# Optimization experiments

Hardware: AMD Instinct MI355X
Metric: run time of the kernel (lower is better)

## Reference

```python
import jax, jax.numpy as jnp
import numpy as np

N0 = 1373      # hardcoded node-type split in the original forward
TAO = 0.4
EPS = 1e-12


def _l2norm(x, axis):
    # matches torch F.normalize(p=2): x / max(||x||, eps)
    n = jnp.sqrt(jnp.sum(x * x, axis=axis, keepdims=True))
    return x / jnp.maximum(n, EPS)


def setup_inputs() -> dict:
    key = jax.random.key(0)
    ks = jax.random.split(key, 12)
    N, E, D_IN, F, H, D = 20000, 320000, 256, 32, 8, 32
    feat = jax.random.normal(ks[0], (N, D_IN), jnp.float32)
    sloc = jax.random.normal(ks[1], (N, D), jnp.float32)
    topo_fea = jax.random.normal(ks[2], (N, D), jnp.float32)
    src = jax.random.randint(ks[3], (E,), 0, N)
    dst = jax.random.randint(ks[4], (E,), 0, N)
    e_feat = jax.random.randint(ks[5], (E,), 0, 4)
    s = 1.0 / np.sqrt(D_IN)
    W_proj0 = jax.random.normal(ks[6], (D_IN, H * F), jnp.float32) * s
    W_proj1 = jax.random.normal(ks[7], (D_IN, H * F), jnp.float32) * s
    W_prob = jax.random.normal(ks[8], (H, F, F), jnp.float32) * (1.0 / np.sqrt(F))
    W_res0 = jax.random.normal(ks[9], (D_IN, H * F), jnp.float32) * s
    W_res1 = jax.random.normal(ks[10], (D_IN, H * F), jnp.float32) * s
    etype_attn = jnp.ones((4,), jnp.float32)
    return dict(feat=feat, sloc=sloc, topo_fea=topo_fea, src=src, dst=dst,
                e_feat=e_feat, W_proj0=W_proj0, W_proj1=W_proj1, W_prob=W_prob,
                W_res0=W_res0, W_res1=W_res1, etype_attn=etype_attn)


def reference(feat, sloc, topo_fea, src, dst, e_feat,
              W_proj0, W_proj1, W_prob, W_res0, W_res1, etype_attn):
    N = feat.shape[0]
    H, F = W_prob.shape[0], W_prob.shape[2]
    sloc3 = sloc[:, None, :]        # (N,1,D) -- .unsqueeze(1)
    topo3 = topo_fea[:, None, :]

    # per-type node projection
    feat_src = jnp.concatenate(
        [feat[:N0] @ W_proj0, feat[N0:] @ W_proj1], axis=0).reshape(N, H, F)
    # per-head attention feature: softmax(tanh(fc4prob_i(.)), dim=feat)
    ft_attn = jax.nn.softmax(
        jnp.tanh(jnp.einsum('nhf,hfg->nhg', feat_src, W_prob)), axis=2)
    # F.normalize over the NODE dimension (dim=0), as in original
    ft_norm = _l2norm(feat_src, axis=0)

    sloc_n = _l2norm(sloc3, axis=2)
    topo_n = _l2norm(topo3, axis=2)

    # edge attention scores
    a = jnp.sum(ft_attn[dst] * ft_norm[src], axis=2, keepdims=True)   # (E,H,1)
    cos_s = jnp.sum(sloc_n[src] * sloc_n[dst], axis=2, keepdims=True)  # (E,1,1)
    cos_t = jnp.sum(topo_n[src] * topo_n[dst], axis=2, keepdims=True)
    sim = (TAO * cos_s + (1.0 - TAO) * cos_t + 1.0) / 2.0             # (E,1,1)
    e = (sim * a * etype_attn[e_feat][:, None, None])[:, :, 0]        # (E,H)

    # edge softmax: segment softmax over incoming edges of each dst node
    m = jax.ops.segment_max(e, dst, num_segments=N)                   # (N,H)
    ex = jnp.exp(e - m[dst])
    z = jax.ops.segment_sum(ex, dst, num_segments=N)
    att = ex / z[dst]                                                 # (E,H)

    # three u_mul_e + sum aggregations
    aw = att[:, :, None]                                              # (E,H,1)
    rst = jax.ops.segment_sum(feat_src[src] * aw, dst, num_segments=N)  # (N,H,F)
    sl2 = jax.ops.segment_sum(sloc3[src] * aw, dst, num_segments=N)     # (N,H,D)
    tp2 = jax.ops.segment_sum(topo3[src] * aw, dst, num_segments=N)     # (N,H,D)

    resval = jnp.concatenate(
        [feat[:N0] @ W_res0, feat[N0:] @ W_res1], axis=0).reshape(N, H, F)
    out_fea = jax.nn.relu(rst + resval).mean(axis=1)   # (N,F)
    out_sloc = (sl2 + sloc3).mean(axis=1)              # (N,D)
    out_topo = (tp2 + topo3).mean(axis=1)              # (N,D)
    return out_fea, out_sloc, out_topo
```

## Files before the change

kernel.cpp:

```cpp
#include <hip/hip_runtime.h>
#include <math.h>

#define HN0 1373
#define BM 128
#define BN 128
#define BK 32
#define LDT 40

typedef __attribute__((ext_vector_type(8))) short short8;
typedef __attribute__((ext_vector_type(4))) float f32x4;

__device__ inline unsigned short f2bf(float f) {
  unsigned int u = __float_as_uint(f);
  unsigned int r = (u + 0x7FFFu + ((u >> 16) & 1u)) >> 16;
  return (unsigned short)r;
}
__device__ inline float bflo(unsigned int u) { return __uint_as_float(u << 16); }
__device__ inline float bfhi(unsigned int u) { return __uint_as_float(u & 0xFFFF0000u); }

__device__ inline uint4 pack8bf(float4 a, float4 b) {
  uint4 o;
  o.x = (unsigned)f2bf(a.x) | ((unsigned)f2bf(a.y) << 16);
  o.y = (unsigned)f2bf(a.z) | ((unsigned)f2bf(a.w) << 16);
  o.z = (unsigned)f2bf(b.x) | ((unsigned)f2bf(b.y) << 16);
  o.w = (unsigned)f2bf(b.z) | ((unsigned)f2bf(b.w) << 16);
  return o;
}

__global__ __launch_bounds__(256) void prep(
    const float* __restrict__ Wp0, const float* __restrict__ Wr0,
    const float* __restrict__ Wp1, const float* __restrict__ Wr1,
    unsigned short* __restrict__ BTw,
    const float* __restrict__ sloc, const float* __restrict__ topo,
    unsigned short* __restrict__ slt, unsigned short* __restrict__ sltn,
    const int* __restrict__ dst, int* __restrict__ deg, int N, int E) {
  __shared__ float T[64][72];
  int b = blockIdx.x;
  int tid = threadIdx.x;
  int nodeBlocks = (N + 7) / 8;
  if (b < 64) {
    int mat = b >> 4;
    int t16 = b & 15;
    int kT = (t16 & 3) * 64;
    int nT = (t16 >> 2) * 64;
    const float* W = (mat == 0) ? Wp0 : (mat == 1) ? Wr0 : (mat == 2) ? Wp1 : Wr1;
    int g = mat >> 1;
    int nbase = (mat & 1) * 256;
    int r = tid >> 2;
    int cb = (tid & 3) * 16;
    const float* srcp = W + (size_t)(kT + r) * 256 + nT + cb;
#pragma unroll
    for (int q = 0; q < 4; ++q) {
      float4 v = *reinterpret_cast<const float4*>(srcp + q * 4);
      T[cb + q * 4 + 0][r] = v.x;
      T[cb + q * 4 + 1][r] = v.y;
      T[cb + q * 4 + 2][r] = v.z;
      T[cb + q * 4 + 3][r] = v.w;
    }
    __syncthreads();
    int nl = tid >> 2;
    int kb = (tid & 3) * 16;
    unsigned int pk[8];
#pragma unroll
    for (int q = 0; q < 8; ++q) {
      unsigned short lo = f2bf(T[nl][kb + q * 2]);
      unsigned short hi = f2bf(T[nl][kb + q * 2 + 1]);
      pk[q] = (unsigned)lo | ((unsigned)hi << 16);
    }
    unsigned short* dstp = BTw + (size_t)g * 512 * 256 + (size_t)(nbase + nT + nl) * 256 + kT + kb;
    *reinterpret_cast<uint4*>(dstp) = make_uint4(pk[0], pk[1], pk[2], pk[3]);
    *reinterpret_cast<uint4*>(dstp + 8) = make_uint4(pk[4], pk[5], pk[6], pk[7]);
  } else if (b < 64 + nodeBlocks) {
    int node = (b - 64) * 8 + (tid >> 5);
    int d = tid & 31;
    if (node >= N) return;
    float s = sloc[(size_t)node * 32 + d];
    float t = topo[(size_t)node * 32 + d];
    float ss = s * s, tt = t * t;
#pragma unroll
    for (int m = 16; m >= 1; m >>= 1) {
      ss += __shfl_xor(ss, m);
      tt += __shfl_xor(tt, m);
    }
    float is = 1.f / fmaxf(sqrtf(ss), 1e-12f);
    float it = 1.f / fmaxf(sqrtf(tt), 1e-12f);
    slt[(size_t)node * 64 + d] = f2bf(s);
    slt[(size_t)node * 64 + 32 + d] = f2bf(t);
    sltn[(size_t)node * 64 + d] = f2bf(s * is);
    sltn[(size_t)node * 64 + 32 + d] = f2bf(t * it);
  } else {
    int e = (b - 64 - nodeBlocks) * 256 + tid;
    if (e < E) atomicAdd(&deg[dst[e]], 1);
  }
}

__global__ __launch_bounds__(256) void gemm_mfma(
    const float* __restrict__ A, const unsigned short* __restrict__ BTw,
    unsigned short* __restrict__ feat_bf, unsigned short* __restrict__ resval,
    int N) {
  __shared__ __align__(16) unsigned short As[BM * LDT];
  __shared__ __align__(16) unsigned short Bs[BN * LDT];
  int tid = threadIdx.x;
  int lane = tid & 63;
  int w = tid >> 6;
  int wr = w >> 1, wc = w & 1;

  int g0t = (HN0 + BM - 1) / BM;
  int bx = blockIdx.x;
  bool g1 = bx >= g0t;
  int rowBase = g1 ? HN0 + (bx - g0t) * BM : bx * BM;
  int rowEnd = g1 ? N : HN0;
  const unsigned short* BT = BTw + (g1 ? (size_t)512 * 256 : 0);
  int colBase = blockIdx.y * BN;

  int r0 = tid >> 2;
  int kp = (tid & 3) << 3;
  int ar1 = min(rowBase + r0, rowEnd - 1);
  int ar2 = min(rowBase + r0 + 64, rowEnd - 1);
  const float* aP1 = A + (size_t)ar1 * 256 + kp;
  const float* aP2 = A + (size_t)ar2 * 256 + kp;
  const unsigned short* bP1 = BT + (size_t)(colBase + r0) * 256 + kp;
  const unsigned short* bP2 = bP1 + (size_t)64 * 256;
  int wo1 = r0 * LDT + kp;
  int wo2 = (r0 + 64) * LDT + kp;

  int q = lane >> 4;
  int fr = lane & 15;
  int aOff = (wr * 64 + fr) * LDT + q * 8;
  int bOff = (wc * 64 + fr) * LDT + q * 8;

  f32x4 acc[4][4] = {};

  float4 fa1a = *reinterpret_cast<const float4*>(aP1);
  float4 fa1b = *reinterpret_cast<const float4*>(aP1 + 4);
  float4 fa2a = *reinterpret_cast<const float4*>(aP2);
  float4 fa2b = *reinterpret_cast<const float4*>(aP2 + 4);
  uint4 rb1 = *reinterpret_cast<const uint4*>(bP1);
  uint4 rb2 = *reinterpret_cast<const uint4*>(bP2);

  for (int t = 0; t < 8; ++t) {
    *reinterpret_cast<uint4*>(&As[wo1]) = pack8bf(fa1a, fa1b);
    *reinterpret_cast<uint4*>(&As[wo2]) = pack8bf(fa2a, fa2b);
    *reinterpret_cast<uint4*>(&Bs[wo1]) = rb1;
    *reinterpret_cast<uint4*>(&Bs[wo2]) = rb2;
    __syncthreads();
    if (t < 7) {
      int ko = (t + 1) * BK;
      fa1a = *reinterpret_cast<const float4*>(aP1 + ko);
      fa1b = *reinterpret_cast<const float4*>(aP1 + ko + 4);
      fa2a = *reinterpret_cast<const float4*>(aP2 + ko);
      fa2b = *reinterpret_cast<const float4*>(aP2 + ko + 4);
      rb1 = *reinterpret_cast<const uint4*>(bP1 + ko);
      rb2 = *reinterpret_cast<const uint4*>(bP2 + ko);
    }
    short8 af[4], bf4[4];
#pragma unroll
    for (int i = 0; i < 4; ++i) {
      af[i] = *reinterpret_cast<const short8*>(&As[aOff + i * 16 * LDT]);
      bf4[i] = *reinterpret_cast<const short8*>(&Bs[bOff + i * 16 * LDT]);
    }
#pragma unroll
    for (int i = 0; i < 4; ++i)
#pragma unroll
      for (int j = 0; j < 4; ++j)
        acc[i][j] = __builtin_amdgcn_mfma_f32_16x16x32_bf16(af[i], bf4[j], acc[i][j], 0, 0, 0);
    __syncthreads();
  }

  unsigned short* outp = (colBase < 256) ? feat_bf : resval;
  int cOff = colBase & 255;
#pragma unroll
  for (int i = 0; i < 4; ++i) {
    int rb = rowBase + wr * 64 + i * 16 + q * 4;
#pragma unroll
    for (int j = 0; j < 4; ++j) {
      int col = cOff + wc * 64 + j * 16 + fr;
      f32x4 v = acc[i][j];
#pragma unroll
      for (int rr = 0; rr < 4; ++rr) {
        int r = rb + rr;
        if (r < rowEnd) outp[(size_t)r * 256 + col] = f2bf(v[rr]);
      }
    }
  }
}

__global__ __launch_bounds__(256) void attn_probs(
    const unsigned short* __restrict__ feat_bf, const float* __restrict__ W_prob,
    unsigned short* __restrict__ ft_attn, float* __restrict__ col_ss, int N) {
  __shared__ float fsL[16 * 256];
  int tid = threadIdx.x;
  int h = tid >> 5, g = tid & 31;
  float wreg[32];
#pragma unroll
  for (int f = 0; f < 32; ++f) wreg[f] = W_prob[h * 1024 + f * 32 + g];
  int nodeBase = blockIdx.x * 16;
  float ssp = 0.f;
  for (int i = 0; i < 16; ++i) {
    int n = nodeBase + i;
    float v = (n < N) ? __uint_as_float((unsigned)feat_bf[(size_t)n * 256 + tid] << 16) : 0.f;
    fsL[i * 256 + tid] = v;
    ssp += v * v;
  }
  atomicAdd(&col_ss[tid], ssp);
  __syncthreads();
  for (int i = 0; i < 16; ++i) {
    int n = nodeBase + i;
    if (n >= N) break;
    const float* fr = &fsL[i * 256 + h * 32];
    float t = 0.f;
#pragma unroll
    for (int f = 0; f < 32; ++f) t = fmaf(fr[f], wreg[f], t);
    float e2 = __expf(2.f * t);
    t = 1.f - 2.f * __builtin_amdgcn_rcpf(e2 + 1.f);
    float ex = __expf(t);
    float sm = ex;
#pragma unroll
    for (int s = 16; s >= 1; s >>= 1) sm += __shfl_xor(sm, s);
    ft_attn[(size_t)n * 256 + tid] = f2bf(ex * __builtin_amdgcn_rcpf(sm));
  }
}

__global__ __launch_bounds__(512) void scan_block(const int* __restrict__ deg,
                                                  int* __restrict__ start,
                                                  int* __restrict__ bsum, int n) {
  __shared__ int buf[512];
  int tid = threadIdx.x;
  int gid = blockIdx.x * 512 + tid;
  int v = (gid < n) ? deg[gid] : 0;
  buf[tid] = v;
  __syncthreads();
  for (int off = 1; off < 512; off <<= 1) {
    int t = (tid >= off) ? buf[tid - off] : 0;
    __syncthreads();
    buf[tid] += t;
    __syncthreads();
  }
  if (gid < n) start[gid] = buf[tid] - v;
  if (tid == 511) bsum[blockIdx.x] = buf[511];
}

__global__ __launch_bounds__(256) void mid_small(float* __restrict__ col_ss,
                                                 int* __restrict__ bsum, int nb) {
  int tid = threadIdx.x;
  col_ss[tid] = 1.f / fmaxf(sqrtf(col_ss[tid]), 1e-12f);
  __shared__ int buf[128];
  if (tid < nb) buf[tid] = bsum[tid];
  __syncthreads();
  if (tid == 0) {
    int run = 0;
    for (int i = 0; i < nb; ++i) { int v = buf[i]; buf[i] = run; run += v; }
  }
  __syncthreads();
  if (tid < nb) bsum[tid] = buf[tid];
}

__global__ __launch_bounds__(256) void fill_sim(
    const int* __restrict__ src, const int* __restrict__ dst,
    const int* __restrict__ e_feat, const float* __restrict__ etype_attn,
    const unsigned short* __restrict__ sltn,
    const int* __restrict__ start, const int* __restrict__ bsum,
    int* __restrict__ cursor, int2* __restrict__ csr, int E) {
  int tid = threadIdx.x;
  int j = tid & 3;
  int e = blockIdx.x * 64 + (tid >> 2);
  if (e >= E) return;
  int s = src[e], d = dst[e];
  const unsigned short* ps = sltn + (size_t)s * 64 + j * 16;
  const unsigned short* pd = sltn + (size_t)d * 64 + j * 16;
  uint4 a0 = *reinterpret_cast<const uint4*>(ps);
  uint4 a1 = *reinterpret_cast<const uint4*>(ps + 8);
  uint4 b0 = *reinterpret_cast<const uint4*>(pd);
  uint4 b1 = *reinterpret_cast<const uint4*>(pd + 8);
  float u = bflo(a0.x) * bflo(b0.x) + bfhi(a0.x) * bfhi(b0.x) +
            bflo(a0.y) * bflo(b0.y) + bfhi(a0.y) * bfhi(b0.y) +
            bflo(a0.z) * bflo(b0.z) + bfhi(a0.z) * bfhi(b0.z) +
            bflo(a0.w) * bflo(b0.w) + bfhi(a0.w) * bfhi(b0.w) +
            bflo(a1.x) * bflo(b1.x) + bfhi(a1.x) * bfhi(b1.x) +
            bflo(a1.y) * bflo(b1.y) + bfhi(a1.y) * bfhi(b1.y) +
            bflo(a1.z) * bflo(b1.z) + bfhi(a1.z) * bfhi(b1.z) +
            bflo(a1.w) * bflo(b1.w) + bfhi(a1.w) * bfhi(b1.w);
  u *= (j < 2) ? 0.4f : 0.6f;
  u += __shfl_xor(u, 1);
  u += __shfl_xor(u, 2);
  if (j == 0) {
    float sim = fmaf(u, 0.5f, 0.5f);
    float wv = sim * etype_attn[e_feat[e]];
    int pos = start[d] + bsum[d >> 9] + atomicAdd(&cursor[d], 1);
    csr[pos] = make_int2(s, __float_as_int(wv));
  }
}

#define LOADIDX(K, V, W)                                                       \
  do {                                                                         \
    int2 c_ = csr[s0 + (K)];                                                   \
    V = c_.x;                                                                  \
    W = __int_as_float(c_.y);                                                  \
  } while (0)

#define GATHER(V, FP, SL, TP)                                                  \
  do {                                                                         \
    FP = *reinterpret_cast<const uint2*>(feat_bf + (size_t)(V) * 256 + fb);    \
    const unsigned short* sp_ = slt + (size_t)(V) * 64 + db;                   \
    SL = *reinterpret_cast<const uint2*>(sp_);                                 \
    TP = *reinterpret_cast<const uint2*>(sp_ + 32);                            \
  } while (0)

#define CONSUME(W, FP, SL, TP)                                                 \
  do {                                                                         \
    float fs0 = bflo(FP.x), fs1 = bfhi(FP.x);                                  \
    float fs2 = bflo(FP.y), fs3 = bfhi(FP.y);                                  \
    float pa = ai4.x * fs0 + ai4.y * fs1 + ai4.z * fs2 + ai4.w * fs3;          \
    pa += __shfl_xor(pa, 1);                                                   \
    pa += __shfl_xor(pa, 2);                                                   \
    pa += __shfl_xor(pa, 4);                                                   \
    float p = __expf(pa * (W));                                                \
    l += p;                                                                    \
    accf.x = fmaf(p, fs0, accf.x); accf.y = fmaf(p, fs1, accf.y);              \
    accf.z = fmaf(p, fs2, accf.z); accf.w = fmaf(p, fs3, accf.w);              \
    accs.x = fmaf(p, bflo(SL.x), accs.x); accs.y = fmaf(p, bfhi(SL.x), accs.y);\
    accs.z = fmaf(p, bflo(SL.y), accs.z); accs.w = fmaf(p, bfhi(SL.y), accs.w);\
    acct.x = fmaf(p, bflo(TP.x), acct.x); acct.y = fmaf(p, bfhi(TP.x), acct.y);\
    acct.z = fmaf(p, bflo(TP.y), acct.z); acct.w = fmaf(p, bfhi(TP.y), acct.w);\
  } while (0)

__global__ __launch_bounds__(128) void edge_aggregate(
    const unsigned short* __restrict__ feat_bf, const unsigned short* __restrict__ resval,
    const unsigned short* __restrict__ ft_attn, const float* __restrict__ inv_cn,
    const unsigned short* __restrict__ slt,
    const float* __restrict__ sloc, const float* __restrict__ topo,
    const int* __restrict__ start, const int* __restrict__ bsum,
    const int* __restrict__ deg, const int2* __restrict__ csr,
    float* __restrict__ out, int N) {
  int wave = threadIdx.x >> 6;
  int n = blockIdx.x * 2 + wave;
  if (n >= N) return;
  int lane = threadIdx.x & 63;
  int j = lane & 7;
  int fb = (lane >> 3) * 32 + j * 4;
  int db = j * 4;

  uint2 at2 = *reinterpret_cast<const uint2*>(ft_attn + (size_t)n * 256 + fb);
  float4 icn4 = *reinterpret_cast<const float4*>(inv_cn + fb);
  float4 ai4 = make_float4(bflo(at2.x) * icn4.x, bfhi(at2.x) * icn4.y,
                           bflo(at2.y) * icn4.z, bfhi(at2.y) * icn4.w);
  float l = 0.f;
  float4 accf = make_float4(0.f, 0.f, 0.f, 0.f);
  float4 accs = make_float4(0.f, 0.f, 0.f, 0.f);
  float4 acct = make_float4(0.f, 0.f, 0.f, 0.f);
  int s0 = start[n] + bsum[n >> 9];
  int dg = deg[n];

  int vA = 0, vB = 0, vC = 0;
  float wA = 0.f, wB = 0.f, wC = 0.f;
  uint2 fpA = make_uint2(0u, 0u), fpB = make_uint2(0u, 0u), fpC = make_uint2(0u, 0u);
  uint2 slA = make_uint2(0u, 0u), slB = make_uint2(0u, 0u), slC = make_uint2(0u, 0u);
  uint2 tpA = make_uint2(0u, 0u), tpB = make_uint2(0u, 0u), tpC = make_uint2(0u, 0u);
  if (dg > 0) { LOADIDX(0, vA, wA); GATHER(vA, fpA, slA, tpA); }
  if (dg > 1) { LOADIDX(1, vB, wB); GATHER(vB, fpB, slB, tpB); }
  if (dg > 2) { LOADIDX(2, vC, wC); GATHER(vC, fpC, slC, tpC); }
  int i = 0;
  for (; i + 2 < dg; i += 3) {
    CONSUME(wA, fpA, slA, tpA);
    if (i + 3 < dg) { LOADIDX(i + 3, vA, wA); GATHER(vA, fpA, slA, tpA); }
    CONSUME(wB, fpB, slB, tpB);
    if (i + 4 < dg) { LOADIDX(i + 4, vB, wB); GATHER(vB, fpB, slB, tpB); }
    CONSUME(wC, fpC, slC, tpC);
    if (i + 5 < dg) { LOADIDX(i + 5, vC, wC); GATHER(vC, fpC, slC, tpC); }
  }
  if (i < dg) CONSUME(wA, fpA, slA, tpA);
  if (i + 1 < dg) CONSUME(wB, fpB, slB, tpB);

  float invl = (l > 0.f) ? 1.f / l : 0.f;

  uint2 res2 = *reinterpret_cast<const uint2*>(resval + (size_t)n * 256 + fb);
  float4 of = make_float4(fmaxf(fmaf(accf.x, invl, bflo(res2.x)), 0.f),
                          fmaxf(fmaf(accf.y, invl, bfhi(res2.x)), 0.f),
                          fmaxf(fmaf(accf.z, invl, bflo(res2.y)), 0.f),
                          fmaxf(fmaf(accf.w, invl, bfhi(res2.y)), 0.f));
  float4 os = make_float4(accs.x * invl, accs.y * invl, accs.z * invl, accs.w * invl);
  float4 ot = make_float4(acct.x * invl, acct.y * invl, acct.z * invl, acct.w * invl);
#pragma unroll
  for (int msk = 8; msk <= 32; msk <<= 1) {
    of.x += __shfl_xor(of.x, msk); of.y += __shfl_xor(of.y, msk);
    of.z += __shfl_xor(of.z, msk); of.w += __shfl_xor(of.w, msk);
    os.x += __shfl_xor(os.x, msk); os.y += __shfl_xor(os.y, msk);
    os.z += __shfl_xor(os.z, msk); os.w += __shfl_xor(os.w, msk);
    ot.x += __shfl_xor(ot.x, msk); ot.y += __shfl_xor(ot.y, msk);
    ot.w += __shfl_xor(ot.w, msk); ot.z += __shfl_xor(ot.z, msk);
  }
  if (lane < 8) {
    float4 sln = *reinterpret_cast<const float4*>(sloc + (size_t)n * 32 + db);
    float4 tpn = *reinterpret_cast<const float4*>(topo + (size_t)n * 32 + db);
    float4 o0 = make_float4(of.x * 0.125f, of.y * 0.125f, of.z * 0.125f, of.w * 0.125f);
    float4 o1 = make_float4(fmaf(os.x, 0.125f, sln.x), fmaf(os.y, 0.125f, sln.y),
                            fmaf(os.z, 0.125f, sln.z), fmaf(os.w, 0.125f, sln.w));
    float4 o2 = make_float4(fmaf(ot.x, 0.125f, tpn.x), fmaf(ot.y, 0.125f, tpn.y),
                            fmaf(ot.z, 0.125f, tpn.z), fmaf(ot.w, 0.125f, tpn.w));
    *reinterpret_cast<float4*>(out + (size_t)n * 32 + db) = o0;
    *reinterpret_cast<float4*>(out + (size_t)N * 32 + (size_t)n * 32 + db) = o1;
    *reinterpret_cast<float4*>(out + (size_t)2 * N * 32 + (size_t)n * 32 + db) = o2;
  }
}

extern "C" void kernel_launch(void* const* d_in, const int* in_sizes, int n_in,
                              void* d_out, int out_size, void* d_ws, size_t ws_size,
                              hipStream_t stream) {
  const float* feat = (const float*)d_in[0];
  const float* sloc = (const float*)d_in[1];
  const float* topo = (const float*)d_in[2];
  const int* src = (const int*)d_in[3];
  const int* dst = (const int*)d_in[4];
  const int* e_feat = (const int*)d_in[5];
  const float* W_proj0 = (const float*)d_in[6];
  const float* W_proj1 = (const float*)d_in[7];
  const float* W_prob = (const float*)d_in[8];
  const float* W_res0 = (const float*)d_in[9];
  const float* W_res1 = (const float*)d_in[10];
  const float* etype_attn = (const float*)d_in[11];
  int E = in_sizes[3];
  int N = in_sizes[1] / 32;
  float* out = (float*)d_out;

  char* ws = (char*)d_ws;
  size_t off = 0;
  auto alloc = [&](size_t bytes) -> char* {
    char* p = ws + off;
    off += (bytes + 255) & ~(size_t)255;
    return p;
  };
  int* deg = (int*)alloc((size_t)N * 4);
  int* cursor = (int*)alloc((size_t)N * 4);
  float* col_ss = (float*)alloc(256 * 4);
  size_t zeroBytes = ((char*)col_ss + 256 * 4) - (char*)deg;
  int* startArr = (int*)alloc(((size_t)N + 1) * 4);
  int* bsum = (int*)alloc(128 * 4);
  int2* csr = (int2*)alloc((size_t)E * 8);
  unsigned short* feat_bf = (unsigned short*)alloc((size_t)N * 256 * 2);
  unsigned short* slt = (unsigned short*)alloc((size_t)N * 64 * 2);
  unsigned short* sltn = (unsigned short*)alloc((size_t)N * 64 * 2);
  unsigned short* resval = (unsigned short*)alloc((size_t)N * 256 * 2);
  unsigned short* ft_attn = (unsigned short*)alloc((size_t)N * 256 * 2);
  unsigned short* BTw = (unsigned short*)alloc((size_t)2 * 512 * 256 * 2);

  hipMemsetAsync(deg, 0, zeroBytes, stream);

  int nodeBlocks = (N + 7) / 8;
  int degBlocks = (E + 255) / 256;
  prep<<<64 + nodeBlocks + degBlocks, 256, 0, stream>>>(
      W_proj0, W_res0, W_proj1, W_res1, BTw, sloc, topo, slt, sltn, dst, deg, N, E);

  int g0t = (HN0 + BM - 1) / BM;
  int g1t = (N - HN0 + BM - 1) / BM;
  gemm_mfma<<<dim3(g0t + g1t, 4), 256, 0, stream>>>(feat, BTw, feat_bf, resval, N);

  attn_probs<<<(N + 15) / 16, 256, 0, stream>>>(feat_bf, W_prob, ft_attn, col_ss, N);

  int nb = (N + 511) / 512;
  scan_block<<<nb, 512, 0, stream>>>(deg, startArr, bsum, N);
  mid_small<<<1, 256, 0, stream>>>(col_ss, bsum, nb);

  fill_sim<<<(E + 63) / 64, 256, 0, stream>>>(src, dst, e_feat, etype_attn, sltn,
                                              startArr, bsum, cursor, csr, E);

  edge_aggregate<<<(N + 1) / 2, 128, 0, stream>>>(feat_bf, resval, ft_attn, col_ss,
                                                  slt, sloc, topo, startArr, bsum,
                                                  deg, csr, out, N);
}
```

Measured before the change: 178.2 us.

## Fold degree scan into GEMM launch and block-sum scan into attention launch

Appends the per-block degree prefix scan (now 256-wide blocks) as extra blocks of the GEMM kernel, and the block-sum exclusive scan as an extra block of the attention-probability kernel. The column-norm reciprocal formerly computed in mid_small is now computed inline in edge_aggregate, and the attention dot product is split into four independent accumulators. This cuts two kernel launches and their serialization gaps, at the cost of redundant per-thread sqrt/reciprocal work and a larger bsum array. The GEMM grid is also flattened to 1D.

```diff
diff --git a/kernel.cpp b/kernel.cpp
--- a/kernel.cpp
+++ b/kernel.cpp
@@ -94,24 +94,43 @@
   }
 }
 
-__global__ __launch_bounds__(256) void gemm_mfma(
+__global__ __launch_bounds__(256) void gemm_scan(
     const float* __restrict__ A, const unsigned short* __restrict__ BTw,
     unsigned short* __restrict__ feat_bf, unsigned short* __restrict__ resval,
-    int N) {
+    const int* __restrict__ deg, int* __restrict__ start, int* __restrict__ bsum,
+    int G, int N) {
+  int b = blockIdx.x;
+  int tid = threadIdx.x;
+  if (b >= G) {
+    __shared__ int buf[256];
+    int b2 = b - G;
+    int gid = b2 * 256 + tid;
+    int v = (gid < N) ? deg[gid] : 0;
+    buf[tid] = v;
+    __syncthreads();
+    for (int off = 1; off < 256; off <<= 1) {
+      int t = (tid >= off) ? buf[tid - off] : 0;
+      __syncthreads();
+      buf[tid] += t;
+      __syncthreads();
+    }
+    if (gid < N) start[gid] = buf[tid] - v;
+    if (tid == 255) bsum[b2] = buf[255];
+    return;
+  }
   __shared__ __align__(16) unsigned short As[BM * LDT];
   __shared__ __align__(16) unsigned short Bs[BN * LDT];
-  int tid = threadIdx.x;
   int lane = tid & 63;
   int w = tid >> 6;
   int wr = w >> 1, wc = w & 1;
 
   int g0t = (HN0 + BM - 1) / BM;
-  int bx = blockIdx.x;
+  int bx = b >> 2;
+  int colBase = (b & 3) * BN;
   bool g1 = bx >= g0t;
   int rowBase = g1 ? HN0 + (bx - g0t) * BM : bx * BM;
   int rowEnd = g1 ? N : HN0;
   const unsigned short* BT = BTw + (g1 ? (size_t)512 * 256 : 0);
-  int colBase = blockIdx.y * BN;
 
   int r0 = tid >> 2;
   int kp = (tid & 3) << 3;
@@ -185,11 +204,24 @@
   }
 }
 
-__global__ __launch_bounds__(256) void attn_probs(
+__global__ __launch_bounds__(256) void attn_mid(
     const unsigned short* __restrict__ feat_bf, const float* __restrict__ W_prob,
-    unsigned short* __restrict__ ft_attn, float* __restrict__ col_ss, int N) {
+    unsigned short* __restrict__ ft_attn, float* __restrict__ col_ss,
+    int* __restrict__ bsum, int nb, int nAttn, int N) {
+  int tid = threadIdx.x;
+  if ((int)blockIdx.x >= nAttn) {
+    __shared__ int buf[128];
+    if (tid < nb) buf[tid] = bsum[tid];
+    __syncthreads();
+    if (tid == 0) {
+      int run = 0;
+      for (int i = 0; i < nb; ++i) { int v = buf[i]; buf[i] = run; run += v; }
+    }
+    __syncthreads();
+    if (tid < nb) bsum[tid] = buf[tid];
+    return;
+  }
   __shared__ float fsL[16 * 256];
-  int tid = threadIdx.x;
   int h = tid >> 5, g = tid & 31;
   float wreg[32];
 #pragma unroll
@@ -208,9 +240,15 @@
     int n = nodeBase + i;
     if (n >= N) break;
     const float* fr = &fsL[i * 256 + h * 32];
-    float t = 0.f;
-#pragma unroll
-    for (int f = 0; f < 32; ++f) t = fmaf(fr[f], wreg[f], t);
+    float t0 = 0.f, t1 = 0.f, t2 = 0.f, t3 = 0.f;
+#pragma unroll
+    for (int f = 0; f < 8; ++f) {
+      t0 = fmaf(fr[f * 4 + 0], wreg[f * 4 + 0], t0);
+      t1 = fmaf(fr[f * 4 + 1], wreg[f * 4 + 1], t1);
+      t2 = fmaf(fr[f * 4 + 2], wreg[f * 4 + 2], t2);
+      t3 = fmaf(fr[f * 4 + 3], wreg[f * 4 + 3], t3);
+    }
+    float t = (t0 + t1) + (t2 + t3);
     float e2 = __expf(2.f * t);
     t = 1.f - 2.f * __builtin_amdgcn_rcpf(e2 + 1.f);
     float ex = __expf(t);
@@ -219,40 +257,6 @@
     for (int s = 16; s >= 1; s >>= 1) sm += __shfl_xor(sm, s);
     ft_attn[(size_t)n * 256 + tid] = f2bf(ex * __builtin_amdgcn_rcpf(sm));
   }
-}
-
-__global__ __launch_bounds__(512) void scan_block(const int* __restrict__ deg,
-                                                  int* __restrict__ start,
-                                                  int* __restrict__ bsum, int n) {
-  __shared__ int buf[512];
-  int tid = threadIdx.x;
-  int gid = blockIdx.x * 512 + tid;
-  int v = (gid < n) ? deg[gid] : 0;
-  buf[tid] = v;
-  __syncthreads();
-  for (int off = 1; off < 512; off <<= 1) {
-    int t = (tid >= off) ? buf[tid - off] : 0;
-    __syncthreads();
-    buf[tid] += t;
-    __syncthreads();
-  }
-  if (gid < n) start[gid] = buf[tid] - v;
-  if (tid == 511) bsum[blockIdx.x] = buf[511];
-}
-
-__global__ __launch_bounds__(256) void mid_small(float* __restrict__ col_ss,
-                                                 int* __restrict__ bsum, int nb) {
-  int tid = threadIdx.x;
-  col_ss[tid] = 1.f / fmaxf(sqrtf(col_ss[tid]), 1e-12f);
-  __shared__ int buf[128];
-  if (tid < nb) buf[tid] = bsum[tid];
-  __syncthreads();
-  if (tid == 0) {
-    int run = 0;
-    for (int i = 0; i < nb; ++i) { int v = buf[i]; buf[i] = run; run += v; }
-  }
-  __syncthreads();
-  if (tid < nb) bsum[tid] = buf[tid];
 }
 
 __global__ __launch_bounds__(256) void fill_sim(
@@ -286,7 +290,7 @@
   if (j == 0) {
     float sim = fmaf(u, 0.5f, 0.5f);
     float wv = sim * etype_attn[e_feat[e]];
-    int pos = start[d] + bsum[d >> 9] + atomicAdd(&cursor[d], 1);
+    int pos = start[d] + bsum[d >> 8] + atomicAdd(&cursor[d], 1);
     csr[pos] = make_int2(s, __float_as_int(wv));
   }
 }
@@ -326,7 +330,7 @@
 
 __global__ __launch_bounds__(128) void edge_aggregate(
     const unsigned short* __restrict__ feat_bf, const unsigned short* __restrict__ resval,
-    const unsigned short* __restrict__ ft_attn, const float* __restrict__ inv_cn,
+    const unsigned short* __restrict__ ft_attn, const float* __restrict__ col_ss,
     const unsigned short* __restrict__ slt,
     const float* __restrict__ sloc, const float* __restrict__ topo,
     const int* __restrict__ start, const int* __restrict__ bsum,
@@ -341,14 +345,18 @@
   int db = j * 4;
 
   uint2 at2 = *reinterpret_cast<const uint2*>(ft_attn + (size_t)n * 256 + fb);
-  float4 icn4 = *reinterpret_cast<const float4*>(inv_cn + fb);
+  float4 cs4 = *reinterpret_cast<const float4*>(col_ss + fb);
+  float4 icn4 = make_float4(1.f / fmaxf(sqrtf(cs4.x), 1e-12f),
+                            1.f / fmaxf(sqrtf(cs4.y), 1e-12f),
+                            1.f / fmaxf(sqrtf(cs4.z), 1e-12f),
+                            1.f / fmaxf(sqrtf(cs4.w), 1e-12f));
   float4 ai4 = make_float4(bflo(at2.x) * icn4.x, bfhi(at2.x) * icn4.y,
                            bflo(at2.y) * icn4.z, bfhi(at2.y) * icn4.w);
   float l = 0.f;
   float4 accf = make_float4(0.f, 0.f, 0.f, 0.f);
   float4 accs = make_float4(0.f, 0.f, 0.f, 0.f);
   float4 acct = make_float4(0.f, 0.f, 0.f, 0.f);
-  int s0 = start[n] + bsum[n >> 9];
+  int s0 = start[n] + bsum[n >> 8];
   int dg = deg[n];
 
   int vA = 0, vB = 0, vC = 0;
@@ -387,7 +395,7 @@
     os.x += __shfl_xor(os.x, msk); os.y += __shfl_xor(os.y, msk);
     os.z += __shfl_xor(os.z, msk); os.w += __shfl_xor(os.w, msk);
     ot.x += __shfl_xor(ot.x, msk); ot.y += __shfl_xor(ot.y, msk);
-    ot.w += __shfl_xor(ot.w, msk); ot.z += __shfl_xor(ot.z, msk);
+    ot.z += __shfl_xor(ot.z, msk); ot.w += __shfl_xor(ot.w, msk);
   }
   if (lane < 8) {
     float4 sln = *reinterpret_cast<const float4*>(sloc + (size_t)n * 32 + db);
@@ -452,13 +460,14 @@
 
   int g0t = (HN0 + BM - 1) / BM;
   int g1t = (N - HN0 + BM - 1) / BM;
-  gemm_mfma<<<dim3(g0t + g1t, 4), 256, 0, stream>>>(feat, BTw, feat_bf, resval, N);
-
-  attn_probs<<<(N + 15) / 16, 256, 0, stream>>>(feat_bf, W_prob, ft_attn, col_ss, N);
-
-  int nb = (N + 511) / 512;
-  scan_block<<<nb, 512, 0, stream>>>(deg, startArr, bsum, N);
-  mid_small<<<1, 256, 0, stream>>>(col_ss, bsum, nb);
+  int G = (g0t + g1t) * 4;
+  int nb = (N + 255) / 256;
+  gemm_scan<<<G + nb, 256, 0, stream>>>(feat, BTw, feat_bf, resval,
+                                        deg, startArr, bsum, G, N);
+
+  int nAttn = (N + 15) / 16;
+  attn_mid<<<nAttn + 1, 256, 0, stream>>>(feat_bf, W_prob, ft_attn, col_ss,
+                                          bsum, nb, nAttn, N);
 
   fill_sim<<<(E + 63) / 64, 256, 0, stream>>>(src, dst, e_feat, etype_attn, sltn,
                                               startArr, bsum, cursor, csr, E);
```

New measurement: 175.3 us. About the same (-1.7%).
